# Kernel optimization log

Hardware: AMD Instinct MI355X
Metric: run time of the kernel (lower is better)

## Reference

```python
import jax, jax.numpy as jnp
import numpy as np

HEADS = 8
DIM_HEAD = 64
ROT_DIM = DIM_HEAD // 2  # RotaryEmbedding(dim=head_dim//2) rotates first 32 dims of each head
THETA = 10000.0


def _rope_cos_sin(T, dtype):
    # rotary_embedding_torch: freqs = 1/theta**(arange(0,dim,2)/dim), len dim//2,
    # angles repeated interleaved across pairs -> (T, ROT_DIM)
    inv = 1.0 / (THETA ** (jnp.arange(0, ROT_DIM, 2, dtype=jnp.float32) / ROT_DIM))
    ang = jnp.arange(T, dtype=jnp.float32)[:, None] * inv[None, :]      # (T, ROT_DIM/2)
    ang = jnp.repeat(ang, 2, axis=-1)                                   # (T, ROT_DIM) interleaved
    return jnp.cos(ang).astype(dtype), jnp.sin(ang).astype(dtype)


def _rotate_half(x):
    # pairs (x1, x2) -> (-x2, x1), interleaved layout '... (d 2)'
    x = x.reshape(x.shape[:-1] + (-1, 2))
    x = jnp.stack([-x[..., 1], x[..., 0]], axis=-1)
    return x.reshape(x.shape[:-2] + (-1,))


def _apply_rope(x, cos, sin):
    # x: (N, h, T, dh); rotate first ROT_DIM dims, pass through the rest
    xr, xp = x[..., :ROT_DIM], x[..., ROT_DIM:]
    xr = xr * cos[None, None, :, :] + _rotate_half(xr) * sin[None, None, :, :]
    return jnp.concatenate([xr, xp], axis=-1)


def setup_inputs() -> dict:
    key = jax.random.key(0)
    k1, k2, k3 = jax.random.split(key, 3)
    B, T, H, W, D = 2, 32, 32, 32, 512
    inner = HEADS * DIM_HEAD
    x = jax.random.normal(k1, (B, T, H, W, D), dtype=jnp.float32)
    w_qkv = jax.random.normal(k2, (D, 3 * inner), dtype=jnp.float32) * (D ** -0.5)
    w_out = jax.random.normal(k3, (inner, D), dtype=jnp.float32) * (inner ** -0.5)
    b_out = jnp.zeros((D,), dtype=jnp.float32)
    return {"x": x, "w_qkv": w_qkv, "w_out": w_out, "b_out": b_out}


def reference(x, w_qkv, w_out, b_out):
    B, T, H, W, D = x.shape
    qkv = jnp.einsum('bthwd,de->bthwe', x, w_qkv)               # (B,T,H,W,3*inner)
    q, k, v = jnp.split(qkv, 3, axis=-1)

    def to_axial(t):  # (B,T,H,W,inner) -> (B*H*W, heads, T, dh)
        t = t.reshape(B, T, H, W, HEADS, DIM_HEAD)
        t = jnp.transpose(t, (0, 2, 3, 4, 1, 5))
        return t.reshape(B * H * W, HEADS, T, DIM_HEAD)

    q, k, v = to_axial(q), to_axial(k), to_axial(v)
    cos, sin = _rope_cos_sin(T, x.dtype)
    q = _apply_rope(q, cos, sin)
    k = _apply_rope(k, cos, sin)

    scale = DIM_HEAD ** -0.5
    scores = jnp.einsum('nhqd,nhkd->nhqk', q, k) * scale        # (N,h,T,T)
    causal = jnp.tril(jnp.ones((T, T), dtype=bool))
    scores = jnp.where(causal[None, None, :, :], scores, jnp.finfo(scores.dtype).min)
    attn = jax.nn.softmax(scores, axis=-1)
    out = jnp.einsum('nhqk,nhkd->nhqd', attn, v)                # (N,h,T,dh)

    out = out.reshape(B, H, W, HEADS, T, DIM_HEAD)
    out = jnp.transpose(out, (0, 4, 1, 2, 3, 5)).reshape(B, T, H, W, HEADS * DIM_HEAD)
    return jnp.einsum('bthwe,ed->bthwd', out, w_out) + b_out
```

## Files before the change

kernel.cpp:

```cpp
#include <hip/hip_runtime.h>
#include <hip/hip_bf16.h>
#include <math.h>

#define HEADS  8
#define TT     32
#define DMODEL 512
#define HWSZ   1024
#define TSTRIDE (HWSZ*DMODEL)

#define NQKV (3*DMODEL*DMODEL)
#define NOUT (DMODEL*DMODEL)
#define NTAB 512

typedef __attribute__((ext_vector_type(8)))  short bf16x8;
typedef __attribute__((ext_vector_type(16))) float f32x16;
typedef __attribute__((ext_vector_type(4)))  short s16x4;
typedef __attribute__((ext_vector_type(2)))  unsigned int u32x2;
typedef __attribute__((ext_vector_type(4)))  unsigned int u32x4;

__device__ __forceinline__ unsigned short f2bf(float f) {
    unsigned int u = __builtin_bit_cast(unsigned int, f);
    u += 0x7FFFu + ((u >> 16) & 1u);
    return (unsigned short)(u >> 16);
}

__device__ __forceinline__ unsigned int pk_bf(float a, float b) {
    return (unsigned int)f2bf(a) | ((unsigned int)f2bf(b) << 16);
}

__device__ __forceinline__ f32x16 fz16() {
    f32x16 v = {0.f,0.f,0.f,0.f,0.f,0.f,0.f,0.f,0.f,0.f,0.f,0.f,0.f,0.f,0.f,0.f};
    return v;
}

__global__ __launch_bounds__(256)
void taa_prep(const float* __restrict__ wqkv, const float* __restrict__ wout,
              unsigned short* __restrict__ ws) {
    long i = (long)blockIdx.x * 256 + threadIdx.x;
    unsigned short* wqf = ws;
    unsigned short* wof = ws + NQKV;
    float* cs = (float*)(wof + NOUT);
    float* sn = cs + NTAB;
    if (i < NQKV) {
        int i8 = (int)(i & 7), lane = (int)((i >> 3) & 63), blk = (int)(i >> 9);
        int k05 = blk & 15, t = blk >> 4;
        int n = t * 16 + (lane & 15);
        int k = k05 * 32 + (lane >> 4) * 8 + i8;
        wqf[i] = f2bf(wqkv[(long)k * 1536 + n]);
    } else if (i < NQKV + NOUT) {
        long j = i - NQKV;
        int i8 = (int)(j & 7), lane = (int)((j >> 3) & 63), blk = (int)(j >> 9);
        int k05 = blk & 15, t = blk >> 4;
        int col = t * 16 + (lane & 15);
        int k = k05 * 32 + (lane >> 4) * 8 + i8;
        wof[j] = f2bf(wout[(long)k * 512 + col]);
    } else if (i < NQKV + NOUT + NTAB) {
        int j = (int)(i - NQKV - NOUT);
        int t = j >> 4, f = j & 15;
        float inv = powf(10000.f, -(float)(2 * f) / 32.f);
        float sv, cv;
        sincosf((float)t * inv, &sv, &cv);
        cs[j] = cv; sn[j] = sv;
    }
}

#define X_OFF  0
#define Q_OFF  65536
#define K_OFF  81920
#define V_OFF  98304
#define PV_OFF 114688
#define CS_OFF 131072
#define SN_OFF 133120
#define LDS_SZ 135168

#define XS(g, r, cB) (X_OFF + ((g) << 15) + ((r) << 10) + ((cB) ^ (((r) & 7) << 4)))
#define RS(base, r, cB) ((base) + ((r) << 7) + ((cB) ^ (((r) & 7) << 4)))
#define VS(base, d, cB) ((base) + ((d) << 6) + ((cB) ^ (((d) & 7) << 3)))

#define MFMA16(a, b, c) __builtin_amdgcn_mfma_f32_16x16x32_bf16((a), (b), (c), 0, 0, 0)
#define MFMA32(a, b, c) __builtin_amdgcn_mfma_f32_32x32x16_bf16((a), (b), (c), 0, 0, 0)

__global__ __launch_bounds__(512, 1)
void taa_main(const float* __restrict__ x,
              const unsigned short* __restrict__ ws,
              const float* __restrict__ b_out,
              float* __restrict__ out) {
    extern __shared__ __align__(16) unsigned char smem[];

    const unsigned short* wqf = ws;
    const unsigned short* wof = ws + NQKV;
    const float* cs_gl = (const float*)(wof + NOUT);
    const float* sn_gl = cs_gl + NTAB;

    const int tid  = threadIdx.x;
    const int lane = tid & 63;
    const int wv   = tid >> 6;
    const int quad = lane >> 4;
    const int lid  = lane & 15;

    const int n0 = blockIdx.x * 2;
    const long long base0 = ((long long)(n0 >> 10) * (TT * HWSZ) + (n0 & 1023)) * DMODEL;
    const int n1 = n0 + 1;
    const long long base1 = ((long long)(n1 >> 10) * (TT * HWSZ) + (n1 & 1023)) * DMODEL;

    float* cs_l = (float*)(smem + CS_OFF);
    float* sn_l = (float*)(smem + SN_OFF);
    for (int i = tid; i < NTAB; i += 512) { cs_l[i] = cs_gl[i]; sn_l[i] = sn_gl[i]; }

    for (int idx = tid; idx < 4096; idx += 512) {
        int g  = idx >> 11;
        int r  = (idx >> 6) & 31;
        int c8 = idx & 63;
        long long bg = g ? base1 : base0;
        const float4* src = (const float4*)(x + bg + (long long)r * TSTRIDE + c8 * 8);
        float4 f0 = src[0], f1 = src[1];
        u32x2 A, B;
        A[0] = pk_bf(f0.x, f0.y); A[1] = pk_bf(f0.z, f0.w);
        B[0] = pk_bf(f1.x, f1.y); B[1] = pk_bf(f1.z, f1.w);
        int a = XS(g, r, c8 * 16);
        *(u32x2*)(smem + a)     = A;
        *(u32x2*)(smem + a + 8) = B;
    }

    typedef __attribute__((ext_vector_type(4))) float f32x4;
    f32x4 oacc[4][2][2];
    #pragma unroll
    for (int j = 0; j < 4; ++j)
        #pragma unroll
        for (int g = 0; g < 2; ++g)
            #pragma unroll
            for (int mt = 0; mt < 2; ++mt) oacc[j][g][mt] = (f32x4){0.f, 0.f, 0.f, 0.f};

    __syncthreads();

    for (int it = 0; it < 4; ++it) {
        const int hpair = it * 2;

        for (int rnd = 0; rnd < 3; ++rnd) {
            int ct  = rnd * 8 + wv;
            int m   = ct >> 3;
            int hh  = (ct >> 2) & 1;
            int t16 = ct & 3;
            int T   = m * 32 + (hpair + hh) * 4 + t16;
            const unsigned short* wp = wqf + ((long)T * 16) * 512 + lane * 8;
            f32x4 acc[2][2];
            #pragma unroll
            for (int g = 0; g < 2; ++g)
                #pragma unroll
                for (int mt = 0; mt < 2; ++mt) acc[g][mt] = (f32x4){0.f, 0.f, 0.f, 0.f};
            #pragma unroll 4
            for (int k05 = 0; k05 < 16; ++k05) {
                bf16x8 bw = *(const bf16x8*)(wp + (long)k05 * 512);
                #pragma unroll
                for (int g = 0; g < 2; ++g)
                    #pragma unroll
                    for (int mt = 0; mt < 2; ++mt) {
                        bf16x8 a = *(const bf16x8*)(smem + XS(g, lid + 16 * mt, k05 * 64 + quad * 16));
                        acc[g][mt] = MFMA16(a, bw, acc[g][mt]);
                    }
            }
            if (m < 2) {
                int dstb = ((m == 0) ? Q_OFF : K_OFF) + hh * 4096;
                if (t16 < 2) {
                    #pragma unroll
                    for (int g = 0; g < 2; ++g)
                        #pragma unroll
                        for (int mt = 0; mt < 2; ++mt)
                            #pragma unroll
                            for (int r = 0; r < 4; ++r) {
                                float v = acc[g][mt][r];
                                float p = __shfl_xor(v, 1, 64);
                                if ((lid & 1) == 0) {
                                    int trow = mt * 16 + quad * 4 + r;
                                    int colh = t16 * 16 + lid;
                                    int jj = colh >> 1;
                                    float cv = cs_l[trow * 16 + jj];
                                    float sv = sn_l[trow * 16 + jj];
                                    float r0 = v * cv - p * sv;
                                    float r1 = p * cv + v * sv;
                                    *(unsigned int*)(smem + RS(dstb + g * 8192, trow, colh * 2)) = pk_bf(r0, r1);
                                }
                            }
                } else {
                    #pragma unroll
                    for (int g = 0; g < 2; ++g)
                        #pragma unroll
                        for (int mt = 0; mt < 2; ++mt)
                            #pragma unroll
                            for (int r = 0; r < 4; ++r) {
                                float v = acc[g][mt][r];
                                float p = __shfl_xor(v, 1, 64);
                                if ((lid & 1) == 0) {
                                    int trow = mt * 16 + quad * 4 + r;
                                    int colh = t16 * 16 + lid;
                                    *(unsigned int*)(smem + RS(dstb + g * 8192, trow, colh * 2)) = pk_bf(v, p);
                                }
                            }
                }
            } else {
                #pragma unroll
                for (int g = 0; g < 2; ++g)
                    #pragma unroll
                    for (int mt = 0; mt < 2; ++mt) {
                        int d  = t16 * 16 + lid;
                        int t0 = mt * 16 + quad * 4;
                        u32x2 pv2;
                        pv2[0] = pk_bf(acc[g][mt][0], acc[g][mt][1]);
                        pv2[1] = pk_bf(acc[g][mt][2], acc[g][mt][3]);
                        *(u32x2*)(smem + VS(V_OFF + (g * 2 + hh) * 4096, d, t0 * 2)) = pv2;
                    }
            }
        }
        __syncthreads();

        {
            int g  = wv >> 2;
            int hh = (wv >> 1) & 1;
            int dt = wv & 1;
            int qr  = Q_OFF  + (g * 2 + hh) * 4096;
            int kr  = K_OFF  + (g * 2 + hh) * 4096;
            int vr  = V_OFF  + (g * 2 + hh) * 4096;
            int pvr = PV_OFF + (g * 2 + hh) * 4096;
            int tq = lane & 31;
            int hf = lane >> 5;

            f32x16 sc = fz16();
            #pragma unroll
            for (int j = 0; j < 4; ++j) {
                bf16x8 aK = *(const bf16x8*)(smem + RS(kr, tq, j * 32 + hf * 16));
                bf16x8 bQ = *(const bf16x8*)(smem + RS(qr, tq, j * 32 + hf * 16));
                sc = MFMA32(aK, bQ, sc);
            }
            float pe[16];
            float mx = -1e30f;
            #pragma unroll
            for (int r = 0; r < 16; ++r) {
                int tk = (r & 3) + 8 * (r >> 2) + 4 * hf;
                float v = (tk <= tq) ? sc[r] * 0.125f : -1e30f;
                pe[r] = v;
                mx = fmaxf(mx, v);
            }
            mx = fmaxf(mx, __shfl_xor(mx, 32, 64));
            float sum = 0.f;
            #pragma unroll
            for (int r = 0; r < 16; ++r) {
                float e = __expf(pe[r] - mx);
                pe[r] = e;
                sum += e;
            }
            sum += __shfl_xor(sum, 32, 64);
            float inv = 1.f / sum;
            u32x4 P0, P1;
            #pragma unroll
            for (int i2 = 0; i2 < 4; ++i2) {
                P0[i2] = pk_bf(pe[2 * i2] * inv,     pe[2 * i2 + 1] * inv);
                P1[i2] = pk_bf(pe[8 + 2 * i2] * inv, pe[9 + 2 * i2] * inv);
            }
            bf16x8 pa0 = __builtin_bit_cast(bf16x8, P0);
            bf16x8 pa1 = __builtin_bit_cast(bf16x8, P1);
            int d = dt * 32 + tq;
            f32x16 o = fz16();
            {
                s16x4 lo = *(const s16x4*)(smem + VS(vr, d, 8 * hf));
                s16x4 hi = *(const s16x4*)(smem + VS(vr, d, 16 + 8 * hf));
                bf16x8 bv;
                bv[0] = lo[0]; bv[1] = lo[1]; bv[2] = lo[2]; bv[3] = lo[3];
                bv[4] = hi[0]; bv[5] = hi[1]; bv[6] = hi[2]; bv[7] = hi[3];
                o = MFMA32(bv, pa0, o);
            }
            {
                s16x4 lo = *(const s16x4*)(smem + VS(vr, d, 32 + 8 * hf));
                s16x4 hi = *(const s16x4*)(smem + VS(vr, d, 48 + 8 * hf));
                bf16x8 bv;
                bv[0] = lo[0]; bv[1] = lo[1]; bv[2] = lo[2]; bv[3] = lo[3];
                bv[4] = hi[0]; bv[5] = hi[1]; bv[6] = hi[2]; bv[7] = hi[3];
                o = MFMA32(bv, pa1, o);
            }
            #pragma unroll
            for (int c = 0; c < 4; ++c) {
                u32x2 pk2;
                pk2[0] = pk_bf(o[4 * c + 0], o[4 * c + 1]);
                pk2[1] = pk_bf(o[4 * c + 2], o[4 * c + 3]);
                int db = dt * 32 + c * 8 + 4 * hf;
                *(u32x2*)(smem + RS(pvr, tq, db * 2)) = pk2;
            }
        }
        __syncthreads();

        {
            #pragma unroll
            for (int k05h = 0; k05h < 4; ++k05h) {
                int hh   = k05h >> 1;
                int dblk = k05h & 1;
                int kb   = (hpair + hh) * 2 + dblk;
                bf16x8 a[2][2];
                #pragma unroll
                for (int g = 0; g < 2; ++g)
                    #pragma unroll
                    for (int mt = 0; mt < 2; ++mt)
                        a[g][mt] = *(const bf16x8*)(smem + RS(PV_OFF + (g * 2 + hh) * 4096, lid + 16 * mt, dblk * 64 + quad * 16));
                #pragma unroll
                for (int j = 0; j < 4; ++j) {
                    int ct = wv + 8 * j;
                    bf16x8 bw = *(const bf16x8*)(wof + ((long)(ct * 16 + kb)) * 512 + lane * 8);
                    #pragma unroll
                    for (int g = 0; g < 2; ++g)
                        #pragma unroll
                        for (int mt = 0; mt < 2; ++mt)
                            oacc[j][g][mt] = MFMA16(a[g][mt], bw, oacc[j][g][mt]);
                }
            }
        }
    }

    #pragma unroll
    for (int j = 0; j < 4; ++j) {
        int col = (wv + 8 * j) * 16 + lid;
        float bias = b_out[col];
        #pragma unroll
        for (int g = 0; g < 2; ++g) {
            long long bg = g ? base1 : base0;
            #pragma unroll
            for (int mt = 0; mt < 2; ++mt)
                #pragma unroll
                for (int r = 0; r < 4; ++r) {
                    int t = mt * 16 + quad * 4 + r;
                    out[bg + (long long)t * TSTRIDE + col] = oacc[j][g][mt][r] + bias;
                }
        }
    }
}

extern "C" void kernel_launch(void* const* d_in, const int* in_sizes, int n_in,
                              void* d_out, int out_size, void* d_ws, size_t ws_size,
                              hipStream_t stream) {
    const float* x     = (const float*)d_in[0];
    const float* w_qkv = (const float*)d_in[1];
    const float* w_out = (const float*)d_in[2];
    const float* b_out = (const float*)d_in[3];
    float* out = (float*)d_out;
    (void)in_sizes; (void)n_in; (void)out_size; (void)ws_size;

    unsigned short* ws = (unsigned short*)d_ws;

    taa_prep<<<dim3(4098), dim3(256), 0, stream>>>(w_qkv, w_out, ws);
    taa_main<<<dim3(1024), dim3(512), LDS_SZ, stream>>>(x, ws, b_out, out);
}
```

Measured before the change: 259.9 us.

## Store X tile in MFMA fragment order and drop shuffles in Q/K/V epilogue

The X tile in LDS is re-laid out so that each lane's 16-byte A fragment for a given k-block and m-tile sits contiguously, with an XOR swizzle on the block index, which simplifies and may de-conflict the MFMA operand loads. The bf16 conversion now uses the HIP intrinsic __float22bfloat162_rn in place of manual rounding bit tricks. In the Q/K epilogue, every lane now computes its own RoPE result and writes a 2-byte bf16 value, removing the divergent branch. In the non-rotated path the cross-lane shuffle is also gone. The trade is twice as many narrower LDS stores, which may add store traffic or bank conflicts.

```diff
diff --git a/kernel.cpp b/kernel.cpp
--- a/kernel.cpp
+++ b/kernel.cpp
@@ -25,7 +25,16 @@
 }
 
 __device__ __forceinline__ unsigned int pk_bf(float a, float b) {
-    return (unsigned int)f2bf(a) | ((unsigned int)f2bf(b) << 16);
+    __hip_bfloat162 h = __float22bfloat162_rn(float2{a, b});
+    unsigned int u;
+    __builtin_memcpy(&u, &h, 4);
+    return u;
+}
+__device__ __forceinline__ unsigned short f2bf_n(float f) {
+    __hip_bfloat16 h = __float2bfloat16(f);
+    unsigned short u;
+    __builtin_memcpy(&u, &h, 2);
+    return u;
 }
 
 __device__ __forceinline__ f32x16 fz16() {
@@ -73,7 +82,7 @@
 #define SN_OFF 133120
 #define LDS_SZ 135168
 
-#define XS(g, r, cB) (X_OFF + ((g) << 15) + ((r) << 10) + ((cB) ^ (((r) & 7) << 4)))
+#define XF(g, blk, ln) (X_OFF + ((g) << 15) + ((blk) << 10) + ((((ln) << 4)) ^ (((blk) & 7) << 4)))
 #define RS(base, r, cB) ((base) + ((r) << 7) + ((cB) ^ (((r) & 7) << 4)))
 #define VS(base, d, cB) ((base) + ((d) << 6) + ((cB) ^ (((d) & 7) << 3)))
 
@@ -114,12 +123,14 @@
         long long bg = g ? base1 : base0;
         const float4* src = (const float4*)(x + bg + (long long)r * TSTRIDE + c8 * 8);
         float4 f0 = src[0], f1 = src[1];
-        u32x2 A, B;
-        A[0] = pk_bf(f0.x, f0.y); A[1] = pk_bf(f0.z, f0.w);
-        B[0] = pk_bf(f1.x, f1.y); B[1] = pk_bf(f1.z, f1.w);
-        int a = XS(g, r, c8 * 16);
-        *(u32x2*)(smem + a)     = A;
-        *(u32x2*)(smem + a + 8) = B;
+        u32x2 lo, hi;
+        lo[0] = pk_bf(f0.x, f0.y); lo[1] = pk_bf(f0.z, f0.w);
+        hi[0] = pk_bf(f1.x, f1.y); hi[1] = pk_bf(f1.z, f1.w);
+        int blk = ((r >> 4) << 4) + (c8 >> 2);
+        int ln  = ((c8 & 3) << 4) | (r & 15);
+        int dest = XF(g, blk, ln);
+        *(u32x2*)(smem + dest)     = lo;
+        *(u32x2*)(smem + dest + 8) = hi;
     }
 
     typedef __attribute__((ext_vector_type(4))) float f32x4;
@@ -155,7 +166,7 @@
                 for (int g = 0; g < 2; ++g)
                     #pragma unroll
                     for (int mt = 0; mt < 2; ++mt) {
-                        bf16x8 a = *(const bf16x8*)(smem + XS(g, lid + 16 * mt, k05 * 64 + quad * 16));
+                        bf16x8 a = *(const bf16x8*)(smem + XF(g, mt * 16 + k05, lane));
                         acc[g][mt] = MFMA16(a, bw, acc[g][mt]);
                     }
             }
@@ -170,16 +181,13 @@
                             for (int r = 0; r < 4; ++r) {
                                 float v = acc[g][mt][r];
                                 float p = __shfl_xor(v, 1, 64);
-                                if ((lid & 1) == 0) {
-                                    int trow = mt * 16 + quad * 4 + r;
-                                    int colh = t16 * 16 + lid;
-                                    int jj = colh >> 1;
-                                    float cv = cs_l[trow * 16 + jj];
-                                    float sv = sn_l[trow * 16 + jj];
-                                    float r0 = v * cv - p * sv;
-                                    float r1 = p * cv + v * sv;
-                                    *(unsigned int*)(smem + RS(dstb + g * 8192, trow, colh * 2)) = pk_bf(r0, r1);
-                                }
+                                int trow = mt * 16 + quad * 4 + r;
+                                int colh = t16 * 16 + lid;
+                                int jj = colh >> 1;
+                                float cv = cs_l[trow * 16 + jj];
+                                float sv = sn_l[trow * 16 + jj];
+                                float res = (colh & 1) ? (v * cv + p * sv) : (v * cv - p * sv);
+                                *(unsigned short*)(smem + RS(dstb + g * 8192, trow, colh * 2)) = f2bf_n(res);
                             }
                 } else {
                     #pragma unroll
@@ -188,13 +196,8 @@
                         for (int mt = 0; mt < 2; ++mt)
                             #pragma unroll
                             for (int r = 0; r < 4; ++r) {
-                                float v = acc[g][mt][r];
-                                float p = __shfl_xor(v, 1, 64);
-                                if ((lid & 1) == 0) {
-                                    int trow = mt * 16 + quad * 4 + r;
-                                    int colh = t16 * 16 + lid;
-                                    *(unsigned int*)(smem + RS(dstb + g * 8192, trow, colh * 2)) = pk_bf(v, p);
-                                }
+                                int trow = mt * 16 + quad * 4 + r;
+                                *(unsigned short*)(smem + RS(dstb + g * 8192, trow, (t16 * 16 + lid) * 2)) = f2bf_n(acc[g][mt][r]);
                             }
                 }
             } else {
```

New measurement: 229.0 us. 1.13x faster.
